# Performance work log

Measured on AMD Instinct MI355X. Metric: run time of the kernel, lower is better.

Reference implementation:

```python
import jax, jax.numpy as jnp
import numpy as np

B, S, D, H = 2, 2048, 2048, 16
HD = D // H  # 128


def _rope_tables(seq_len, half_dim, theta=10000.0):
    freqs = 1.0 / (theta ** (np.arange(0, half_dim, dtype=np.float32) / half_dim))
    t = np.arange(seq_len, dtype=np.float32)
    ang = np.outer(t, freqs)  # [S, HD//2]
    return jnp.asarray(np.cos(ang)), jnp.asarray(np.sin(ang))


def setup_inputs() -> dict:
    key = jax.random.key(0)
    kx, kq, kk, kv, ko = jax.random.split(key, 5)
    cos, sin = _rope_tables(S, HD // 2)
    return {
        "x": jax.random.normal(kx, (B, S, D), dtype=jnp.float32),
        "cos": cos,  # [S, HD//2]
        "sin": sin,  # [S, HD//2]
        "wq": jax.random.normal(kq, (D, D), dtype=jnp.float32) * 0.02,
        "wk": jax.random.normal(kk, (D, D), dtype=jnp.float32) * 0.02,
        "wv": jax.random.normal(kv, (D, D), dtype=jnp.float32) * 0.02,
        "wo": jax.random.normal(ko, (D, D), dtype=jnp.float32) * 0.02,
    }


def _apply_rotary(t, cos, sin):
    # t: [B, S, H, HD]; rotate consecutive pairs (complex multiply)
    t2 = t.reshape(*t.shape[:-1], HD // 2, 2)
    te, to = t2[..., 0], t2[..., 1]
    c = cos[None, :, None, :]
    s = sin[None, :, None, :]
    out = jnp.stack([te * c - to * s, te * s + to * c], axis=-1)
    return out.reshape(t.shape)


def reference(x, cos, sin, wq, wk, wv, wo):
    xq = (x @ wq).reshape(B, S, H, HD)
    xk = (x @ wk).reshape(B, S, H, HD)
    xv = (x @ wv).reshape(B, S, H, HD)
    # FAITHFUL to source: rotary applied to xq and xv (NOT xk)
    xq = _apply_rotary(xq, cos, sin)
    xv = _apply_rotary(xv, cos, sin)
    q = xq.transpose(0, 2, 1, 3)  # [B,H,S,HD]
    k = xk.transpose(0, 2, 1, 3)
    v = xv.transpose(0, 2, 1, 3)
    scores = jnp.einsum("bhqd,bhkd->bhqk", q, k) / jnp.sqrt(jnp.float32(HD))
    mask = jnp.triu(jnp.full((S, S), -jnp.inf, dtype=scores.dtype), k=1)
    scores = scores + mask[None, None, :, :]
    probs = jax.nn.softmax(scores, axis=-1)
    out = jnp.einsum("bhqk,bhkd->bhqd", probs, v)  # [B,H,S,HD]
    out = out.transpose(0, 2, 1, 3).reshape(B, S, D)
    return out @ wo
```

## Files before the change

kernel.cpp:

```cpp
#include <hip/hip_runtime.h>
#include <hip/hip_bf16.h>

typedef short short8 __attribute__((ext_vector_type(8)));
typedef float f32x4 __attribute__((ext_vector_type(4)));
typedef int int4v __attribute__((ext_vector_type(4)));

#define B_ 2
#define S_ 2048
#define D_ 2048
#define H_ 16
#define HD_ 128
#define K_ 2048

#define GLL16(gp, lp) __builtin_amdgcn_global_load_lds( \
    (const __attribute__((address_space(1))) void*)(gp), \
    (__attribute__((address_space(3))) void*)(lp), 16, 0, 0)

__device__ inline ushort f2bf(float f) {
    union { float f; unsigned u; } v; v.f = f;
    unsigned r = v.u + 0x7FFFu + ((v.u >> 16) & 1u);
    return (ushort)(r >> 16);
}
__device__ inline float bf2f(ushort b) {
    union { unsigned u; float f; } v; v.u = ((unsigned)b) << 16;
    return v.f;
}

__global__ void cast_kernel(const float* __restrict__ src, ushort* __restrict__ dst, int n4) {
    int i = blockIdx.x * blockDim.x + threadIdx.x;
    if (i >= n4) return;
    float4 v = reinterpret_cast<const float4*>(src)[i];
    ushort4 o;
    o.x = f2bf(v.x); o.y = f2bf(v.y); o.z = f2bf(v.z); o.w = f2bf(v.w);
    reinterpret_cast<ushort4*>(dst)[i] = o;
}

__global__ __launch_bounds__(256) void cast_transpose4(
        const float* __restrict__ s0, const float* __restrict__ s1,
        const float* __restrict__ s2, const float* __restrict__ s3,
        ushort* __restrict__ d0, ushort* __restrict__ d1,
        ushort* __restrict__ d2, ushort* __restrict__ d3) {
    __shared__ ushort tile[64][72];
    const int z = blockIdx.z;
    const float* src = (z == 0) ? s0 : (z == 1) ? s1 : (z == 2) ? s2 : s3;
    ushort* dst = (z == 0) ? d0 : (z == 1) ? d1 : (z == 2) ? d2 : d3;
    const int bk = blockIdx.y * 64, bn = blockIdx.x * 64;
    const int t = threadIdx.x;
    #pragma unroll
    for (int it = 0; it < 4; ++it) {
        int id = t + it * 256;
        int row = id >> 4;
        int c4 = (id & 15) * 4;
        float4 v = *reinterpret_cast<const float4*>(&src[(size_t)(bk + row) * D_ + bn + c4]);
        ushort4 o; o.x = f2bf(v.x); o.y = f2bf(v.y); o.z = f2bf(v.z); o.w = f2bf(v.w);
        *reinterpret_cast<ushort4*>(&tile[row][c4]) = o;
    }
    __syncthreads();
    #pragma unroll
    for (int it = 0; it < 4; ++it) {
        int id = t + it * 256;
        int n = id >> 4;
        int c4 = (id & 15) * 4;
        ushort4 o;
        o.x = tile[c4 + 0][n]; o.y = tile[c4 + 1][n];
        o.z = tile[c4 + 2][n]; o.w = tile[c4 + 3][n];
        *reinterpret_cast<ushort4*>(&dst[(size_t)(bn + n) * D_ + bk + c4]) = o;
    }
}

#define BAR8() __builtin_amdgcn_s_barrier()
#define VMC0() asm volatile("s_waitcnt vmcnt(0)" ::: "memory")

template<int MODE>
__global__ __launch_bounds__(512, 2) void gemm8(const ushort* __restrict__ A,
        const ushort* __restrict__ Bt, ushort* __restrict__ q0, ushort* __restrict__ k0,
        ushort* __restrict__ v0, float* __restrict__ outf,
        const float* __restrict__ cosT, const float* __restrict__ sinT, int nbx) {
    constexpr int NC      = (MODE == 0) ? 4 : 2;
    constexpr int BN      = (MODE == 0) ? 256 : 128;
    constexpr int BHROWS  = BN / 2;
    constexpr int BHBYTES = BHROWS * 128;
    constexpr int BSTRIDE = 32768 + 2 * BHBYTES;
    constexpr int WROWS   = BHROWS / 2;

    extern __shared__ char smem[];
    const int tid = threadIdx.x, lane = tid & 63, wv = tid >> 6;
    const int wm = wv >> 2, wn = wv & 3;
    const int l15 = lane & 15, lg = lane >> 4;
    const int nwg = (int)gridDim.x, cpx = nwg >> 3;
    const int swzb = ((int)blockIdx.x & 7) * cpx + ((int)blockIdx.x >> 3);
    const int bn = (swzb % nbx) * BN, bm = (swzb / nbx) * 256;

    f32x4 acc[8][NC] = {};

    const int grl = wv * 8 + (lane >> 3);
    const int swc = (((lane & 7) ^ ((lane >> 3) & 7)) * 8);
    const ushort* Ag = A + (size_t)(bm + grl) * K_ + swc;
    const ushort* Bg = Bt + (size_t)(bn + grl) * K_ + swc;
    const size_t rowHA = (size_t)128 * K_;
    const size_t rowHB = (size_t)BHROWS * K_;
    const size_t row64 = (size_t)64 * K_;

#define VMC() do { if (MODE == 0) asm volatile("s_waitcnt vmcnt(2)" ::: "memory"); \
                   else           asm volatile("s_waitcnt vmcnt(1)" ::: "memory"); } while (0)
#define STAGE_A(t, h) do { if ((t) < 32) { \
        const ushort* g = Ag + (size_t)(h) * rowHA + (size_t)(t) * 64; \
        char* l = smem + (((t) & 1) ? BSTRIDE : 0) + ((h) << 14) + (wv << 10); \
        GLL16(g, l); GLL16(g + row64, l + 8192); } } while (0)
#define STAGE_B(t, h) do { if ((t) < 32) { \
        const ushort* g = Bg + (size_t)(h) * rowHB + (size_t)(t) * 64; \
        char* l = smem + (((t) & 1) ? BSTRIDE : 0) + 32768 + (h) * BHBYTES + (wv << 10); \
        GLL16(g, l); if (MODE == 0) GLL16(g + row64, l + 8192); } } while (0)

    const int colsw0 = (lg * 16) ^ ((l15 & 7) << 4);
    const int colsw1 = (64 + lg * 16) ^ ((l15 & 7) << 4);
    const char* abase0 = smem + (wm << 14);
    const char* bbase0 = smem + 32768 + (wn >> 1) * BHBYTES;
    const char* abase1 = abase0 + BSTRIDE;
    const char* bbase1 = bbase0 + BSTRIDE;
    const int brow = ((wn & 1) * WROWS + l15) * 128;

#define LDA(ab, q, cs) do { _Pragma("unroll") for (int f = 0; f < 4; ++f) \
        a[f] = *reinterpret_cast<const short8*>((ab) + ((q) * 64 + f * 16 + l15) * 128 + (cs)); } while (0)
#define LDB(bb, cs) do { _Pragma("unroll") for (int c = 0; c < NC; ++c) \
        b[c] = *reinterpret_cast<const short8*>((bb) + brow + c * 2048 + (cs)); } while (0)
#define MM(q) do { __builtin_amdgcn_s_setprio(1); \
        _Pragma("unroll") for (int f = 0; f < 4; ++f) \
        _Pragma("unroll") for (int c = 0; c < NC; ++c) \
            acc[(q) * 4 + f][c] = __builtin_amdgcn_mfma_f32_16x16x32_bf16(a[f], b[c], acc[(q) * 4 + f][c], 0, 0, 0); \
        __builtin_amdgcn_s_setprio(0); } while (0)

    STAGE_A(0, 0); STAGE_A(0, 1); STAGE_B(0, 0); STAGE_B(0, 1);
    STAGE_B(1, 0);
    VMC();
    BAR8();

    for (int i = 0; i < 16; ++i) {
        const int t1 = 2 * i + 1, s0 = 2 * i + 2, s1 = 2 * i + 3;
        short8 a[4], b[NC];
        LDB(bbase0, colsw0); LDA(abase0, 0, colsw0);
        STAGE_A(t1, 0);
        BAR8(); MM(0); BAR8();
        LDA(abase0, 1, colsw0);
        STAGE_A(t1, 1);
        BAR8(); MM(1); BAR8();
        LDB(bbase0, colsw1); LDA(abase0, 0, colsw1);
        STAGE_B(t1, 1);
        BAR8(); MM(0); BAR8();
        LDA(abase0, 1, colsw1);
        STAGE_B(s0, 0);
        if (s0 < 32) VMC(); else VMC0();
        BAR8(); MM(1); BAR8();
        LDB(bbase1, colsw0); LDA(abase1, 0, colsw0);
        STAGE_A(s0, 0);
        BAR8(); MM(0); BAR8();
        LDA(abase1, 1, colsw0);
        STAGE_A(s0, 1);
        BAR8(); MM(1); BAR8();
        LDB(bbase1, colsw1); LDA(abase1, 0, colsw1);
        STAGE_B(s0, 1);
        BAR8(); MM(0); BAR8();
        LDA(abase1, 1, colsw1);
        STAGE_B(s1, 0);
        if (s1 < 32) VMC(); else VMC0();
        BAR8(); MM(1); BAR8();
    }

    const int colbase = bn + wn * (BN / 4);
    if (MODE == 0) {
        const int seg = colbase >> 11;
        ushort* segp = (seg == 0) ? q0 : ((seg == 1) ? k0 : v0);
        const bool dorope = (seg != 1);
        const int dbase = colbase & 127;
        #pragma unroll
        for (int rf = 0; rf < 8; ++rf)
            #pragma unroll
            for (int c = 0; c < NC; ++c) {
                const int d = dbase + c * 16 + l15;
                const int ih = d >> 1;
                #pragma unroll
                for (int j = 0; j < 4; ++j) {
                    int row = bm + wm * 128 + rf * 16 + lg * 4 + j;
                    int col = colbase + c * 16 + l15;
                    int bb = row >> 11, s = row & (S_ - 1);
                    int h = (col >> 7) & (H_ - 1);
                    float v = acc[rf][c][j];
                    float outv;
                    if (dorope) {
                        float vp = __shfl_xor(v, 1);
                        float cs = cosT[s * 64 + ih], sn = sinT[s * 64 + ih];
                        outv = (l15 & 1) ? fmaf(vp, sn, v * cs) : fmaf(v, cs, -(vp * sn));
                    } else {
                        outv = v;
                    }
                    segp[(((size_t)(bb * H_ + h)) * S_ + s) * HD_ + d] = f2bf(outv);
                }
            }
    } else {
        #pragma unroll
        for (int rf = 0; rf < 8; ++rf)
            #pragma unroll
            for (int c = 0; c < NC; ++c)
                #pragma unroll
                for (int j = 0; j < 4; ++j) {
                    int row = bm + wm * 128 + rf * 16 + lg * 4 + j;
                    int col = colbase + c * 16 + l15;
                    outf[(size_t)row * D_ + col] = acc[rf][c][j];
                }
    }
#undef VMC
#undef STAGE_A
#undef STAGE_B
#undef LDA
#undef LDB
#undef MM
}

__global__ __launch_bounds__(512, 4) void attn5(const ushort* __restrict__ Qm,
        const ushort* __restrict__ Km, const ushort* __restrict__ Vm,
        ushort* __restrict__ Om) {
    __shared__ __align__(16) ushort Kb[2][64 * 128];
    __shared__ __align__(16) ushort Vt[2][128][72];
    const int tid = threadIdx.x, lane = tid & 63, wv = tid >> 6;
    const int l15 = lane & 15, lg = lane >> 4;
    const int yy = (int)blockIdx.y;
    const int qt = (yy < 8) ? (15 - 2 * yy) : (2 * (yy - 8));
    const int bh = blockIdx.x;
    const size_t base = (size_t)bh * S_ * HD_;
    const int qrow0 = qt * 128 + wv * 16;
    const float C = 0.1275174f;

    short8 qf[4];
    {
        const ushort* qp = Qm + base + (size_t)(qrow0 + l15) * HD_;
        #pragma unroll
        for (int c = 0; c < 4; ++c)
            qf[c] = *reinterpret_cast<const short8*>(qp + c * 32 + lg * 8);
    }
    f32x4 oacc[8] = {};
    float mS = -1e30f, lS = 0.f;
    const int ntiles = 2 * qt + 2;
    const int kmask0 = 2 * qt + (wv >> 2);

    {
        #pragma unroll
        for (int c = 0; c < 2; ++c) {
            int row = wv * 8 + c * 4 + (lane >> 4);
            GLL16(Km + base + (size_t)row * HD_ + (((lane & 15) ^ (row & 7)) << 3),
                  &Kb[0][wv * 1024 + c * 512]);
        }
        const ushort* vp = Vm + base + (size_t)lane * HD_ + wv * 16;
        #pragma unroll
        for (int cc = 0; cc < 2; ++cc) {
            int4v v = *reinterpret_cast<const int4v*>(vp + cc * 8);
            const ushort* e = reinterpret_cast<const ushort*>(&v);
            #pragma unroll
            for (int j = 0; j < 8; ++j) Vt[0][wv * 16 + cc * 8 + j][lane] = e[j];
        }
    }
    __syncthreads();

    int cur = 0;
    for (int kt = 0; kt < ntiles; ++kt) {
        const bool pfn = (kt + 1 < ntiles);
        int4v vr[2];
        if (pfn) {
            const int r0 = (kt + 1) * 64;
            #pragma unroll
            for (int c = 0; c < 2; ++c) {
                int row = wv * 8 + c * 4 + (lane >> 4);
                GLL16(Km + base + (size_t)(r0 + row) * HD_ + (((lane & 15) ^ (row & 7)) << 3),
                      &Kb[cur ^ 1][wv * 1024 + c * 512]);
            }
            const ushort* vp = Vm + base + (size_t)(r0 + lane) * HD_ + wv * 16;
            #pragma unroll
            for (int cc = 0; cc < 2; ++cc)
                vr[cc] = *reinterpret_cast<const int4v*>(vp + cc * 8);
        }
        f32x4 sacc[4] = {};
        const ushort* Kc = &Kb[cur][0];
        __builtin_amdgcn_s_setprio(1);
        #pragma unroll
        for (int ct = 0; ct < 4; ++ct) {
            const int row = ct * 16 + l15;
            const int sw = (row & 7) << 3;
            #pragma unroll
            for (int c = 0; c < 4; ++c) {
                short8 kf = *reinterpret_cast<const short8*>(
                    Kc + row * 128 + ((c * 32 + lg * 8) ^ sw));
                sacc[ct] = __builtin_amdgcn_mfma_f32_16x16x32_bf16(kf, qf[c], sacc[ct], 0, 0, 0);
            }
        }
        __builtin_amdgcn_s_setprio(0);

        float t16[16];
        #pragma unroll
        for (int ct = 0; ct < 4; ++ct)
            #pragma unroll
            for (int j = 0; j < 4; ++j) t16[ct * 4 + j] = sacc[ct][j];
        if (kt >= kmask0) {
            const int thr = qrow0 + l15 - kt * 64;
            #pragma unroll
            for (int ct = 0; ct < 4; ++ct)
                #pragma unroll
                for (int j = 0; j < 4; ++j)
                    if (ct * 16 + lg * 4 + j > thr) t16[ct * 4 + j] = -1e30f;
        }
        float mx[8];
        #pragma unroll
        for (int i = 0; i < 8; ++i) mx[i] = fmaxf(t16[i], t16[i + 8]);
        #pragma unroll
        for (int i = 0; i < 4; ++i) mx[i] = fmaxf(mx[i], mx[i + 4]);
        float m64 = fmaxf(fmaxf(mx[0], mx[1]), fmaxf(mx[2], mx[3]));
        m64 = fmaxf(m64, __shfl_xor(m64, 16));
        m64 = fmaxf(m64, __shfl_xor(m64, 32));
        if (!__all(m64 - mS <= 47.0f)) {
            float mnew = fmaxf(mS, m64);
            float corr = __builtin_amdgcn_exp2f((mS - mnew) * C);
            lS *= corr;
            #pragma unroll
            for (int dt = 0; dt < 8; ++dt)
                #pragma unroll
                for (int j = 0; j < 4; ++j) oacc[dt][j] *= corr;
            mS = mnew;
        }
        const float mcc = mS * C;
        float p[16];
        #pragma unroll
        for (int i = 0; i < 16; ++i)
            p[i] = __builtin_amdgcn_exp2f(fmaf(t16[i], C, -mcc));
        float sm[8];
        #pragma unroll
        for (int i = 0; i < 8; ++i) sm[i] = p[i] + p[i + 8];
        #pragma unroll
        for (int i = 0; i < 4; ++i) sm[i] = sm[i] + sm[i + 4];
        float psum = (sm[0] + sm[1]) + (sm[2] + sm[3]);
        psum += __shfl_xor(psum, 16);
        psum += __shfl_xor(psum, 32);
        lS += psum;

        unsigned dw[8];
        #pragma unroll
        for (int ct = 0; ct < 4; ++ct)
            #pragma unroll
            for (int u = 0; u < 2; ++u) {
                __hip_bfloat162 h2 = __float22bfloat162_rn(
                    float2{p[ct * 4 + 2 * u], p[ct * 4 + 2 * u + 1]});
                dw[ct * 2 + u] = *reinterpret_cast<unsigned*>(&h2);
            }
        #pragma unroll
        for (int c2 = 0; c2 < 2; ++c2) {
            int4v pfd;
            #pragma unroll
            for (int d = 0; d < 4; ++d) {
                int srcl = (lg & 1) * 32 + (d >> 1) * 16 + l15;
                int r0 = __shfl((int)dw[(2 * c2) * 2 + (d & 1)], srcl);
                int r1 = __shfl((int)dw[(2 * c2 + 1) * 2 + (d & 1)], srcl);
                pfd[d] = (lg & 2) ? r1 : r0;
            }
            short8 pf = *reinterpret_cast<short8*>(&pfd);
            __builtin_amdgcn_s_setprio(1);
            #pragma unroll
            for (int dt = 0; dt < 8; ++dt) {
                short8 vf = *reinterpret_cast<const short8*>(
                    &Vt[cur][dt * 16 + l15][c2 * 32 + lg * 8]);
                oacc[dt] = __builtin_amdgcn_mfma_f32_16x16x32_bf16(vf, pf, oacc[dt], 0, 0, 0);
            }
            __builtin_amdgcn_s_setprio(0);
        }
        if (pfn) {
            #pragma unroll
            for (int cc = 0; cc < 2; ++cc) {
                const ushort* e = reinterpret_cast<const ushort*>(&vr[cc]);
                #pragma unroll
                for (int j = 0; j < 8; ++j) Vt[cur ^ 1][wv * 16 + cc * 8 + j][lane] = e[j];
            }
        }
        __syncthreads();
        cur ^= 1;
    }
    const int b = bh >> 4, h = bh & (H_ - 1);
    const int q = qrow0 + l15;
    const float inv = 1.0f / lS;
    ushort* op = Om + ((size_t)(b * S_ + q)) * D_ + h * HD_;
    #pragma unroll
    for (int dt = 0; dt < 8; ++dt) {
        ushort4 o;
        o.x = f2bf(oacc[dt][0] * inv);
        o.y = f2bf(oacc[dt][1] * inv);
        o.z = f2bf(oacc[dt][2] * inv);
        o.w = f2bf(oacc[dt][3] * inv);
        *reinterpret_cast<ushort4*>(op + dt * 16 + lg * 4) = o;
    }
}

extern "C" void kernel_launch(void* const* d_in, const int* in_sizes, int n_in,
                              void* d_out, int out_size, void* d_ws, size_t ws_size,
                              hipStream_t stream) {
    const float* x    = (const float*)d_in[0];
    const float* cosT = (const float*)d_in[1];
    const float* sinT = (const float*)d_in[2];
    const float* wq   = (const float*)d_in[3];
    const float* wk   = (const float*)d_in[4];
    const float* wv   = (const float*)d_in[5];
    const float* wo   = (const float*)d_in[6];
    float* out = (float*)d_out;

    char* ws = (char*)d_ws;
    const size_t szX = (size_t)B_ * S_ * D_ * 2;
    const size_t szW = (size_t)D_ * D_ * 2;
    ushort* xb   = (ushort*)(ws);
    ushort* wcat = (ushort*)(ws + szX);
    ushort* woT  = (ushort*)(ws + szX + 3 * szW);
    ushort* q0   = (ushort*)(ws + szX + 4 * szW);
    ushort* k0   = (ushort*)(ws + szX + 4 * szW + szX);
    ushort* v0   = (ushort*)(ws + szX + 4 * szW + 2 * szX);
    ushort* att  = xb;

    hipFuncSetAttribute(reinterpret_cast<const void*>(&gemm8<0>),
                        hipFuncAttributeMaxDynamicSharedMemorySize, 131072);
    hipFuncSetAttribute(reinterpret_cast<const void*>(&gemm8<1>),
                        hipFuncAttributeMaxDynamicSharedMemorySize, 98304);

    const int nx = B_ * S_ * D_;
    cast_kernel<<<nx / 4 / 256, 256, 0, stream>>>(x, xb, nx / 4);
    cast_transpose4<<<dim3(D_ / 64, D_ / 64, 4), 256, 0, stream>>>(
        wq, wk, wv, wo, wcat, wcat + (size_t)D_ * D_, wcat + 2 * (size_t)D_ * D_, woT);

    gemm8<0><<<384, 512, 131072, stream>>>(xb, wcat, q0, k0, v0, nullptr, cosT, sinT, 24);

    attn5<<<dim3(B_ * H_, S_ / 128), 512, 0, stream>>>(q0, k0, v0, att);

    gemm8<1><<<256, 512, 98304, stream>>>(att, woT, nullptr, nullptr, nullptr, out,
                                          nullptr, nullptr, 16);
}
```

Before: 292.8 us.

## Retile QKV GEMM to 192-wide columns and move rotary into separate kernels

The QKV projection GEMM now uses a 256x192 output tile, so the launch has 512 workgroups instead of 384. At two workgroups per CU this loads every CU evenly. The B-tile staging and LDS layout are rewritten into 64-row chunks, and the wait counts are adjusted to match. Because a 192-wide tile can straddle head and segment boundaries, the rotary embedding is removed from the GEMM epilogue and applied by two standalone elementwise kernels on q and v. Those kernels add an extra read and write pass over both tensors.

New measurement: 265.2 us. 1.1x faster.

```diff
diff --git a/kernel.cpp b/kernel.cpp
--- a/kernel.cpp
+++ b/kernel.cpp
@@ -68,20 +68,36 @@
     }
 }
 
+__global__ void rope_kernel(ushort* __restrict__ t, const float* __restrict__ cosT,
+                            const float* __restrict__ sinT, int npairs) {
+    int pid = blockIdx.x * blockDim.x + threadIdx.x;
+    if (pid >= npairs) return;
+    int i = pid & 63;
+    int s = (pid >> 6) & (S_ - 1);
+    unsigned pr = reinterpret_cast<unsigned*>(t)[pid];
+    float e = bf2f((ushort)(pr & 0xFFFFu));
+    float o = bf2f((ushort)(pr >> 16));
+    float c = cosT[s * 64 + i];
+    float sn = sinT[s * 64 + i];
+    float oe = e * c - o * sn;
+    float oo = e * sn + o * c;
+    unsigned outp = ((unsigned)f2bf(oo) << 16) | (unsigned)f2bf(oe);
+    reinterpret_cast<unsigned*>(t)[pid] = outp;
+}
+
 #define BAR8() __builtin_amdgcn_s_barrier()
+#define VMC1() asm volatile("s_waitcnt vmcnt(1)" ::: "memory")
 #define VMC0() asm volatile("s_waitcnt vmcnt(0)" ::: "memory")
 
 template<int MODE>
 __global__ __launch_bounds__(512, 2) void gemm8(const ushort* __restrict__ A,
         const ushort* __restrict__ Bt, ushort* __restrict__ q0, ushort* __restrict__ k0,
-        ushort* __restrict__ v0, float* __restrict__ outf,
-        const float* __restrict__ cosT, const float* __restrict__ sinT, int nbx) {
-    constexpr int NC      = (MODE == 0) ? 4 : 2;
-    constexpr int BN      = (MODE == 0) ? 256 : 128;
-    constexpr int BHROWS  = BN / 2;
-    constexpr int BHBYTES = BHROWS * 128;
-    constexpr int BSTRIDE = 32768 + 2 * BHBYTES;
-    constexpr int WROWS   = BHROWS / 2;
+        ushort* __restrict__ v0, float* __restrict__ outf, int nbx) {
+    constexpr int NC      = (MODE == 0) ? 3 : 2;
+    constexpr int BN      = (MODE == 0) ? 192 : 128;
+    constexpr int WCOLS   = BN / 4;
+    constexpr int BBYTES  = BN * 128;
+    constexpr int BSTRIDE = 32768 + BBYTES;
 
     extern __shared__ char smem[];
     const int tid = threadIdx.x, lane = tid & 63, wv = tid >> 6;
@@ -98,41 +114,40 @@
     const ushort* Ag = A + (size_t)(bm + grl) * K_ + swc;
     const ushort* Bg = Bt + (size_t)(bn + grl) * K_ + swc;
     const size_t rowHA = (size_t)128 * K_;
-    const size_t rowHB = (size_t)BHROWS * K_;
     const size_t row64 = (size_t)64 * K_;
 
-#define VMC() do { if (MODE == 0) asm volatile("s_waitcnt vmcnt(2)" ::: "memory"); \
-                   else           asm volatile("s_waitcnt vmcnt(1)" ::: "memory"); } while (0)
 #define STAGE_A(t, h) do { if ((t) < 32) { \
         const ushort* g = Ag + (size_t)(h) * rowHA + (size_t)(t) * 64; \
         char* l = smem + (((t) & 1) ? BSTRIDE : 0) + ((h) << 14) + (wv << 10); \
         GLL16(g, l); GLL16(g + row64, l + 8192); } } while (0)
-#define STAGE_B(t, h) do { if ((t) < 32) { \
-        const ushort* g = Bg + (size_t)(h) * rowHB + (size_t)(t) * 64; \
-        char* l = smem + (((t) & 1) ? BSTRIDE : 0) + 32768 + (h) * BHBYTES + (wv << 10); \
-        GLL16(g, l); if (MODE == 0) GLL16(g + row64, l + 8192); } } while (0)
+#define STAGE_B(t, ch) do { if ((t) < 32) { \
+        const ushort* g = Bg + (size_t)(ch) * row64 + (size_t)(t) * 64; \
+        char* l = smem + (((t) & 1) ? BSTRIDE : 0) + 32768 + (ch) * 8192 + (wv << 10); \
+        GLL16(g, l); } } while (0)
+#define STAGE_B_HI(t) do { STAGE_B(t, 1); if (MODE == 0) STAGE_B(t, 2); } while (0)
 
     const int colsw0 = (lg * 16) ^ ((l15 & 7) << 4);
     const int colsw1 = (64 + lg * 16) ^ ((l15 & 7) << 4);
     const char* abase0 = smem + (wm << 14);
-    const char* bbase0 = smem + 32768 + (wn >> 1) * BHBYTES;
+    const char* bbase0 = smem + 32768;
     const char* abase1 = abase0 + BSTRIDE;
     const char* bbase1 = bbase0 + BSTRIDE;
-    const int brow = ((wn & 1) * WROWS + l15) * 128;
 
 #define LDA(ab, q, cs) do { _Pragma("unroll") for (int f = 0; f < 4; ++f) \
         a[f] = *reinterpret_cast<const short8*>((ab) + ((q) * 64 + f * 16 + l15) * 128 + (cs)); } while (0)
-#define LDB(bb, cs) do { _Pragma("unroll") for (int c = 0; c < NC; ++c) \
-        b[c] = *reinterpret_cast<const short8*>((bb) + brow + c * 2048 + (cs)); } while (0)
+#define LDB(bb, cs) do { _Pragma("unroll") for (int c = 0; c < NC; ++c) { \
+        const int rw = wn * WCOLS + c * 16; \
+        b[c] = *reinterpret_cast<const short8*>((bb) + (rw >> 6) * 8192 + ((rw & 63) + l15) * 128 + (cs)); } } while (0)
 #define MM(q) do { __builtin_amdgcn_s_setprio(1); \
         _Pragma("unroll") for (int f = 0; f < 4; ++f) \
         _Pragma("unroll") for (int c = 0; c < NC; ++c) \
             acc[(q) * 4 + f][c] = __builtin_amdgcn_mfma_f32_16x16x32_bf16(a[f], b[c], acc[(q) * 4 + f][c], 0, 0, 0); \
         __builtin_amdgcn_s_setprio(0); } while (0)
 
-    STAGE_A(0, 0); STAGE_A(0, 1); STAGE_B(0, 0); STAGE_B(0, 1);
+    STAGE_A(0, 0); STAGE_A(0, 1);
+    STAGE_B(0, 0); STAGE_B_HI(0);
     STAGE_B(1, 0);
-    VMC();
+    VMC1();
     BAR8();
 
     for (int i = 0; i < 16; ++i) {
@@ -145,11 +160,11 @@
         STAGE_A(t1, 1);
         BAR8(); MM(1); BAR8();
         LDB(bbase0, colsw1); LDA(abase0, 0, colsw1);
-        STAGE_B(t1, 1);
+        STAGE_B_HI(t1);
         BAR8(); MM(0); BAR8();
         LDA(abase0, 1, colsw1);
         STAGE_B(s0, 0);
-        if (s0 < 32) VMC(); else VMC0();
+        if (s0 < 32) VMC1(); else VMC0();
         BAR8(); MM(1); BAR8();
         LDB(bbase1, colsw0); LDA(abase1, 0, colsw0);
         STAGE_A(s0, 0);
@@ -158,44 +173,31 @@
         STAGE_A(s0, 1);
         BAR8(); MM(1); BAR8();
         LDB(bbase1, colsw1); LDA(abase1, 0, colsw1);
-        STAGE_B(s0, 1);
+        STAGE_B_HI(s0);
         BAR8(); MM(0); BAR8();
         LDA(abase1, 1, colsw1);
         STAGE_B(s1, 0);
-        if (s1 < 32) VMC(); else VMC0();
+        if (s1 < 32) VMC1(); else VMC0();
         BAR8(); MM(1); BAR8();
     }
 
-    const int colbase = bn + wn * (BN / 4);
     if (MODE == 0) {
-        const int seg = colbase >> 11;
-        ushort* segp = (seg == 0) ? q0 : ((seg == 1) ? k0 : v0);
-        const bool dorope = (seg != 1);
-        const int dbase = colbase & 127;
-        #pragma unroll
-        for (int rf = 0; rf < 8; ++rf)
-            #pragma unroll
-            for (int c = 0; c < NC; ++c) {
-                const int d = dbase + c * 16 + l15;
-                const int ih = d >> 1;
+        #pragma unroll
+        for (int c = 0; c < NC; ++c) {
+            const int col0 = bn + wn * WCOLS + c * 16;
+            const int seg = col0 >> 11;
+            ushort* segp = (seg == 0) ? q0 : ((seg == 1) ? k0 : v0);
+            const int col = col0 + l15;
+            const int h = (col >> 7) & (H_ - 1), d = col & (HD_ - 1);
+            #pragma unroll
+            for (int rf = 0; rf < 8; ++rf)
                 #pragma unroll
                 for (int j = 0; j < 4; ++j) {
                     int row = bm + wm * 128 + rf * 16 + lg * 4 + j;
-                    int col = colbase + c * 16 + l15;
                     int bb = row >> 11, s = row & (S_ - 1);
-                    int h = (col >> 7) & (H_ - 1);
-                    float v = acc[rf][c][j];
-                    float outv;
-                    if (dorope) {
-                        float vp = __shfl_xor(v, 1);
-                        float cs = cosT[s * 64 + ih], sn = sinT[s * 64 + ih];
-                        outv = (l15 & 1) ? fmaf(vp, sn, v * cs) : fmaf(v, cs, -(vp * sn));
-                    } else {
-                        outv = v;
-                    }
-                    segp[(((size_t)(bb * H_ + h)) * S_ + s) * HD_ + d] = f2bf(outv);
+                    segp[(((size_t)(bb * H_ + h)) * S_ + s) * HD_ + d] = f2bf(acc[rf][c][j]);
                 }
-            }
+        }
     } else {
         #pragma unroll
         for (int rf = 0; rf < 8; ++rf)
@@ -204,13 +206,13 @@
                 #pragma unroll
                 for (int j = 0; j < 4; ++j) {
                     int row = bm + wm * 128 + rf * 16 + lg * 4 + j;
-                    int col = colbase + c * 16 + l15;
+                    int col = bn + wn * WCOLS + c * 16 + l15;
                     outf[(size_t)row * D_ + col] = acc[rf][c][j];
                 }
     }
-#undef VMC
 #undef STAGE_A
 #undef STAGE_B
+#undef STAGE_B_HI
 #undef LDA
 #undef LDB
 #undef MM
@@ -418,7 +420,7 @@
     ushort* att  = xb;
 
     hipFuncSetAttribute(reinterpret_cast<const void*>(&gemm8<0>),
-                        hipFuncAttributeMaxDynamicSharedMemorySize, 131072);
+                        hipFuncAttributeMaxDynamicSharedMemorySize, 114688);
     hipFuncSetAttribute(reinterpret_cast<const void*>(&gemm8<1>),
                         hipFuncAttributeMaxDynamicSharedMemorySize, 98304);
 
@@ -427,10 +429,13 @@
     cast_transpose4<<<dim3(D_ / 64, D_ / 64, 4), 256, 0, stream>>>(
         wq, wk, wv, wo, wcat, wcat + (size_t)D_ * D_, wcat + 2 * (size_t)D_ * D_, woT);
 
-    gemm8<0><<<384, 512, 131072, stream>>>(xb, wcat, q0, k0, v0, nullptr, cosT, sinT, 24);
+    gemm8<0><<<512, 512, 114688, stream>>>(xb, wcat, q0, k0, v0, nullptr, 32);
+
+    const int npairs = B_ * S_ * H_ * 64;
+    rope_kernel<<<npairs / 256, 256, 0, stream>>>(q0, cosT, sinT, npairs);
+    rope_kernel<<<npairs / 256, 256, 0, stream>>>(v0, cosT, sinT, npairs);
 
     attn5<<<dim3(B_ * H_, S_ / 128), 512, 0, stream>>>(q0, k0, v0, att);
 
-    gemm8<1><<<256, 512, 98304, stream>>>(att, woT, nullptr, nullptr, nullptr, out,
-                                          nullptr, nullptr, 16);
-}
+    gemm8<1><<<256, 512, 98304, stream>>>(att, woT, nullptr, nullptr, nullptr, out, 16);
+}
```
